# Kernel tuning notes

Hardware: AMD Instinct MI355X
Metric: run time of the kernel (lower is better)

## Reference

```python
import jax, jax.numpy as jnp
import numpy as np

WARP_WEIGHT = 2.5   # level 2
MD = 3              # max displacement -> 7x7 = 49 correlation channels
NEG_SLOPE = 0.1


def setup_inputs() -> dict:
    key = jax.random.key(0)
    ks = jax.random.split(key, 9)
    B, C, H, W = 8, 128, 128, 128
    features1 = jax.random.normal(ks[0], (B, C, H, W), jnp.float32)
    features2 = jax.random.normal(ks[1], (B, C, H, W), jnp.float32)
    flow = jax.random.normal(ks[2], (B, 2, H // 2, W // 2), jnp.float32)

    def conv_w(k, o, i, kh, kw):
        bound = 1.0 / np.sqrt(i * kh * kw)
        return jax.random.uniform(k, (o, i, kh, kw), jnp.float32, -bound, bound)

    def conv_b(k, o, i, kh, kw):
        bound = 1.0 / np.sqrt(i * kh * kw)
        return jax.random.uniform(k, (o,), jnp.float32, -bound, bound)

    return {
        "features1": features1,
        "features2": features2,
        "flow": flow,
        "w1": conv_w(ks[3], 64, 49, 3, 3), "b1": conv_b(ks[4], 64, 49, 3, 3),
        "w2": conv_w(ks[5], 32, 64, 3, 3), "b2": conv_b(ks[6], 32, 64, 3, 3),
        "w3": conv_w(ks[7], 2, 32, 5, 5),  "b3": conv_b(ks[8], 2, 32, 5, 5),
    }


def _resize_bilinear(x, h, w):
    # matches torch interpolate(mode='bilinear', align_corners=False)
    B, C = x.shape[:2]
    return jax.image.resize(x, (B, C, h, w), method="bilinear")


def _warp(img, fl):
    # backward warp: sample img at (x + fl_x, y + fl_y), bilinear, zeros outside
    B, C, H, W = img.shape
    yy, xx = jnp.meshgrid(jnp.arange(H, dtype=jnp.float32),
                          jnp.arange(W, dtype=jnp.float32), indexing="ij")
    x = xx[None] + fl[:, 0]   # [B,H,W]
    y = yy[None] + fl[:, 1]
    x0f, y0f = jnp.floor(x), jnp.floor(y)
    wx, wy = x - x0f, y - y0f
    x0, y0 = x0f.astype(jnp.int32), y0f.astype(jnp.int32)

    def gather(yi, xi):
        valid = (yi >= 0) & (yi < H) & (xi >= 0) & (xi < W)
        yc = jnp.clip(yi, 0, H - 1)
        xc = jnp.clip(xi, 0, W - 1)
        v = jax.vmap(lambda im, a, b: im[:, a, b])(img, yc, xc)  # [B,C,H,W]
        return v * valid[:, None].astype(img.dtype)

    return (gather(y0, x0) * ((1 - wx) * (1 - wy))[:, None]
            + gather(y0, x0 + 1) * (wx * (1 - wy))[:, None]
            + gather(y0 + 1, x0) * ((1 - wx) * wy)[:, None]
            + gather(y0 + 1, x0 + 1) * (wx * wy)[:, None])


def _correlation(f1, f2):
    # windowed cost volume: out[b, dy*7+dx] = mean_c f1[b,c,y,x]*f2[b,c,y+dy-3,x+dx-3]
    B, C, H, W = f1.shape
    f2p = jnp.pad(f2, ((0, 0), (0, 0), (MD, MD), (MD, MD)))
    outs = [jnp.mean(f1 * f2p[:, :, dy:dy + H, dx:dx + W], axis=1)
            for dy in range(2 * MD + 1) for dx in range(2 * MD + 1)]
    return jnp.stack(outs, axis=1)  # [B,49,H,W]


def _conv(x, w, b, pad):
    y = jax.lax.conv_general_dilated(
        x, w, window_strides=(1, 1), padding=[(pad, pad), (pad, pad)],
        dimension_numbers=("NCHW", "OIHW", "NCHW"))
    return y + b[None, :, None, None]


def _lrelu(x):
    return jnp.where(x >= 0, x, NEG_SLOPE * x)


def reference(features1, features2, flow, w1, b1, w2, b2, w3, b3):
    H, W = features1.shape[-2:]
    flow_up = _resize_bilinear(flow, H, W)                 # [B,2,H,W]
    f2w = _warp(features2, flow_up * WARP_WEIGHT)
    corr = _correlation(features1, f2w)                    # [B,49,H,W]
    h = _lrelu(_conv(corr, w1, b1, 1))
    h = _lrelu(_conv(h, w2, b2, 1))
    h = _conv(h, w3, b3, 2)                                # [B,2,H,W]
    return flow_up + h
```

## Files before the change

### kernel.cpp

```cpp
#include <hip/hip_runtime.h>
#include <hip/hip_bf16.h>

#define BB 8
#define CC 128
#define HH 128
#define WW 128
#define HW (HH*WW)
#define MD 3
#define ND 49
#define WARP_WEIGHT 2.5f
#define NEG 0.1f

typedef __attribute__((ext_vector_type(8))) short bf16x8;
typedef __attribute__((ext_vector_type(4))) float f32x4;

__device__ inline ushort f2bf(float f) {
    __hip_bfloat16 h = __float2bfloat16(f);
    return *reinterpret_cast<ushort*>(&h);
}
__device__ inline float bf2f(short s) {
    return __uint_as_float(((uint)(ushort)s) << 16);
}

#define G8_IDX(b, y, g) ((((size_t)((b) * HH + (y)) * 16) + (g)) * (WW * 8))

__global__ void k_flow_up(const float* __restrict__ flow, float* __restrict__ flow_up) {
    const int x = threadIdx.x;
    const int y = blockIdx.x;
    const int c = blockIdx.y;
    const int b = blockIdx.z;
    const int Hs = 64, Ws = 64;
    float sy = (y + 0.5f) * 0.5f - 0.5f;
    float sx = (x + 0.5f) * 0.5f - 0.5f;
    float y0f = floorf(sy), x0f = floorf(sx);
    int y0 = (int)y0f, x0 = (int)x0f;
    float wy = sy - y0f, wx = sx - x0f;
    int y0c = min(max(y0, 0), Hs - 1), y1c = min(max(y0 + 1, 0), Hs - 1);
    int x0c = min(max(x0, 0), Ws - 1), x1c = min(max(x0 + 1, 0), Ws - 1);
    const float* src = flow + ((size_t)(b * 2 + c)) * Hs * Ws;
    float v00 = src[y0c * Ws + x0c], v01 = src[y0c * Ws + x1c];
    float v10 = src[y1c * Ws + x0c], v11 = src[y1c * Ws + x1c];
    float v = v00 * (1.f - wx) * (1.f - wy) + v01 * wx * (1.f - wy)
            + v10 * (1.f - wx) * wy + v11 * wx * wy;
    flow_up[((size_t)(b * 2 + c) * HH + y) * WW + x] = v;
}

__global__ __launch_bounds__(256) void k_prep_cl(const float* __restrict__ src,
                                                 ushort* __restrict__ dstcl) {
    __shared__ ushort lds[128][68];
    const int y = blockIdx.x & 127;
    const int b = (blockIdx.x >> 7) & 7;
    const int chunk = blockIdx.x >> 10;
    {
        const int x = threadIdx.x & 127;
        const int cg = threadIdx.x >> 7;
        const int c0 = chunk * 64 + cg * 32;
        const float* s = src + ((size_t)b * CC + c0) * HW + y * WW + x;
#pragma unroll
        for (int j4 = 0; j4 < 8; j4++) {
            ushort t[4];
#pragma unroll
            for (int u = 0; u < 4; u++) t[u] = f2bf(s[(size_t)(j4 * 4 + u) * HW]);
            *reinterpret_cast<uint2*>(&lds[x][cg * 32 + j4 * 4]) =
                *reinterpret_cast<const uint2*>(t);
        }
    }
    __syncthreads();
    {
        const int xw = threadIdx.x >> 1;
        const int h = threadIdx.x & 1;
        ushort* d = dstcl + (((size_t)(b * HH + y)) * WW + xw) * CC + chunk * 64 + h * 32;
#pragma unroll
        for (int i = 0; i < 8; i++)
            *reinterpret_cast<uint2*>(d + i * 4) =
                *reinterpret_cast<const uint2*>(&lds[xw][h * 32 + i * 4]);
    }
}

__global__ __launch_bounds__(256) void k_warp2(const ushort* __restrict__ f2cl,
                                               const float* __restrict__ flow_up,
                                               ushort* __restrict__ f2wg8) {
    const int bid = blockIdx.x;
    const int k = bid & 7;
    const int t = bid >> 3;
    const int xs = t & 7;
    const int y  = k * 16 + ((t >> 3) & 15);
    const int b  = t >> 7;
    const int p  = threadIdx.x >> 4;
    const int g  = threadIdx.x & 15;
    const int x  = xs * 16 + p;

    const float fx = flow_up[((size_t)(b * 2 + 0) * HH + y) * WW + x] * WARP_WEIGHT;
    const float fy = flow_up[((size_t)(b * 2 + 1) * HH + y) * WW + x] * WARP_WEIGHT;
    const float sx = (float)x + fx;
    const float sy = (float)y + fy;
    float x0f = floorf(sx), y0f = floorf(sy);
    int x0 = (int)x0f, y0 = (int)y0f;
    float wx = sx - x0f, wy = sy - y0f;
    int x0c = min(max(x0, 0), WW - 1), x1c = min(max(x0 + 1, 0), WW - 1);
    int y0c = min(max(y0, 0), HH - 1), y1c = min(max(y0 + 1, 0), HH - 1);
    bool vx0 = (x0 >= 0) & (x0 < WW);
    bool vx1 = (x0 + 1 >= 0) & (x0 + 1 < WW);
    bool vy0 = (y0 >= 0) & (y0 < HH);
    bool vy1 = (y0 + 1 >= 0) & (y0 + 1 < HH);
    float w00 = (vx0 && vy0) ? (1.f - wx) * (1.f - wy) : 0.f;
    float w01 = (vx1 && vy0) ? wx * (1.f - wy) : 0.f;
    float w10 = (vx0 && vy1) ? (1.f - wx) * wy : 0.f;
    float w11 = (vx1 && vy1) ? wx * wy : 0.f;

    const ushort* base = f2cl + (size_t)b * HW * CC + (size_t)g * 8;
    bf16x8 t00 = *reinterpret_cast<const bf16x8*>(base + ((size_t)y0c * WW + x0c) * CC);
    bf16x8 t01 = *reinterpret_cast<const bf16x8*>(base + ((size_t)y0c * WW + x1c) * CC);
    bf16x8 t10 = *reinterpret_cast<const bf16x8*>(base + ((size_t)y1c * WW + x0c) * CC);
    bf16x8 t11 = *reinterpret_cast<const bf16x8*>(base + ((size_t)y1c * WW + x1c) * CC);

    ushort o[8];
#pragma unroll
    for (int j = 0; j < 8; j++) {
        float v = w00 * bf2f(t00[j]) + w01 * bf2f(t01[j])
                + w10 * bf2f(t10[j]) + w11 * bf2f(t11[j]);
        o[j] = f2bf(v);
    }
    *reinterpret_cast<uint4*>(f2wg8 + G8_IDX(b, y, g) + x * 8) =
        *reinterpret_cast<const uint4*>(o);
}

__global__ __launch_bounds__(512, 4) void k_corr_mfma(const float* __restrict__ f1,
                                                      const ushort* __restrict__ f2g8,
                                                      ushort* __restrict__ Ct) {
    __shared__ ushort cstage[128][68];
    const int b  = blockIdx.x & 7;
    const int y  = blockIdx.x >> 3;
    const int w  = threadIdx.x >> 6;
    const int l  = threadIdx.x & 63;
    const int lx = l & 15;
    const int lk = l >> 4;
    const int xa0 = w * 16;

    const int xb0 = xa0 - 3 + lx;
    const int xb1 = xa0 + 13 + lx;
    const int xc0 = min(max(xb0, 0), WW - 1);
    const int xc1 = min(max(xb1, 0), WW - 1);
    const bool xm0 = (unsigned)xb0 < (unsigned)WW;
    const bool xm1 = (unsigned)xb1 < (unsigned)WW;
    const bf16x8 zf = {};

    bf16x8 bb[2][8];
    auto load_b = [&](int dy, int buf) {
        const int yy = y + dy - MD;
        const bool yv = (unsigned)yy < (unsigned)HH;
        const int yc = min(max(yy, 0), HH - 1);
#pragma unroll
        for (int kk = 0; kk < 4; kk++) {
            const ushort* grp = f2g8 + G8_IDX(b, yc, kk * 4 + lk);
            bf16x8 b0 = *reinterpret_cast<const bf16x8*>(grp + xc0 * 8);
            bf16x8 b1 = *reinterpret_cast<const bf16x8*>(grp + xc1 * 8);
            bb[buf][kk * 2 + 0] = (yv && xm0) ? b0 : zf;
            bb[buf][kk * 2 + 1] = (yv && xm1) ? b1 : zf;
        }
    };

    load_b(0, 0);
    load_b(1, 1);

    bf16x8 afr[4];
#pragma unroll
    for (int kk = 0; kk < 4; kk++) {
        const float* src = f1 + ((size_t)(b * CC + kk * 32 + lk * 8)) * HW
                         + y * WW + xa0 + lx;
        float tv[8];
#pragma unroll
        for (int j = 0; j < 8; j++) tv[j] = src[(size_t)j * HW];
        ushort tmp[8];
#pragma unroll
        for (int j = 0; j < 8; j++) tmp[j] = f2bf(tv[j]);
        afr[kk] = *reinterpret_cast<const bf16x8*>(tmp);
    }

    const float scale = 1.f / (float)CC;

#pragma unroll
    for (int dy = 0; dy < 7; dy++) {
        f32x4 acc0 = (f32x4)(0.f), acc1 = (f32x4)(0.f);
#pragma unroll
        for (int kk = 0; kk < 4; kk++) {
            acc0 = __builtin_amdgcn_mfma_f32_16x16x32_bf16(
                afr[kk], bb[dy & 1][kk * 2 + 0], acc0, 0, 0, 0);
            acc1 = __builtin_amdgcn_mfma_f32_16x16x32_bf16(
                afr[kk], bb[dy & 1][kk * 2 + 1], acc1, 0, 0, 0);
        }
        if (dy + 2 < 7) load_b(dy + 2, dy & 1);
#pragma unroll
        for (int r = 0; r < 4; r++) {
            const int i = lk * 4 + r;
            const int d0 = lx - i;
            if (d0 >= 0 && d0 <= 6)
                cstage[xa0 + i][dy * 7 + d0] = f2bf(acc0[r] * scale);
            const int d1 = lx - i + 16;
            if (d1 >= 0 && d1 <= 6)
                cstage[xa0 + i][dy * 7 + d1] = f2bf(acc1[r] * scale);
        }
    }

    {
        const int row = xa0 + (l >> 2);
        const int part = l & 3;
        ushort* dst = Ct + (((size_t)(b * HH + y)) * WW + row) * 64 + part * 16;
        if (part < 3) {
            uint2 t0 = *reinterpret_cast<const uint2*>(&cstage[row][part * 16 + 0]);
            uint2 t1 = *reinterpret_cast<const uint2*>(&cstage[row][part * 16 + 4]);
            uint2 t2 = *reinterpret_cast<const uint2*>(&cstage[row][part * 16 + 8]);
            uint2 t3 = *reinterpret_cast<const uint2*>(&cstage[row][part * 16 + 12]);
            uint4 v0; v0.x = t0.x; v0.y = t0.y; v0.z = t1.x; v0.w = t1.y;
            uint4 v1; v1.x = t2.x; v1.y = t2.y; v1.z = t3.x; v1.w = t3.y;
            *reinterpret_cast<uint4*>(dst) = v0;
            *reinterpret_cast<uint4*>(dst + 8) = v1;
        } else {
            uint4 v0; v0.x = (uint)cstage[row][48]; v0.y = 0u; v0.z = 0u; v0.w = 0u;
            uint4 v1; v1.x = 0u; v1.y = 0u; v1.z = 0u; v1.w = 0u;
            *reinterpret_cast<uint4*>(dst) = v0;
            *reinterpret_cast<uint4*>(dst + 8) = v1;
        }
    }
}

template<int IC, int ICP, int OC, int OCP, int KK>
__global__ void k_prep_w2(const float* __restrict__ w, ushort* __restrict__ Wt) {
    constexpr int NCH = ICP / 32;
    int e = blockIdx.x * 256 + threadIdx.x;
    const int total = KK * KK * NCH * 4 * OCP * 8;
    if (e >= total) return;
    int j  = e & 7;
    int oc = (e >> 3) % OCP;
    int lk = (e / (8 * OCP)) & 3;
    int t  = e / (8 * OCP * 4);
    int ch = t % NCH;
    int tap = t / NCH;
    int kh = tap / KK, kw = tap % KK;
    int c = ch * 32 + lk * 8 + j;
    float v = 0.f;
    if (oc < OC && c < IC) v = w[((oc * IC + c) * KK + kh) * KK + kw];
    Wt[e] = f2bf(v);
}

template<int ICP, int OCP, int MT, int NT, int OCOUT, int KK, int PAD, bool RELU, bool LAST>
__global__ __launch_bounds__(512, 4) void k_conv_lds(
    const ushort* __restrict__ In, const ushort* __restrict__ Wt,
    const float* __restrict__ bias, ushort* __restrict__ Out,
    const float* __restrict__ flow_up, float* __restrict__ fout)
{
    constexpr int NCH = ICP / 32;
    constexpr int NTAP = KK * KK * NCH;
    constexpr int ROWB = ICP * 2;
    constexpr int ROWBYTES = WW * ROWB;
    constexpr int NROWS = KK + 1;
    constexpr int SLAB = NROWS * ROWBYTES;
    constexpr int LOG2ROWB = (ICP == 64) ? 7 : 6;
    constexpr int SWZM = (ICP == 64) ? 7 : 3;
    constexpr int ITER = SLAB / (512 * 16);

    __shared__ __align__(16) char slds[SLAB];

    const int y0 = blockIdx.x * 2;
    const int b = blockIdx.y;
    const char* inb = (const char*)(In + (size_t)b * HH * WW * ICP);

#pragma unroll
    for (int it = 0; it < ITER; it++) {
        int L = it * 512 * 16 + threadIdx.x * 16;
        int r = L / ROWBYTES;
        int Lr = L % ROWBYTES;
        int grow = min(max(y0 - PAD + r, 0), HH - 1);
        uint4 v = *reinterpret_cast<const uint4*>(inb + (size_t)grow * ROWBYTES + Lr);
        int dst = r * ROWBYTES + (Lr ^ (((Lr >> LOG2ROWB) & SWZM) << 4));
        *reinterpret_cast<uint4*>(&slds[dst]) = v;
    }
    __syncthreads();

    const int w = threadIdx.x >> 6;
    const int l = threadIdx.x & 63;
    const int lx = l & 15;
    const int lk = l >> 4;
    const int wr = w >> 2;
    const int wq = w & 3;
    const int y = y0 + wr;
    const int n0 = wq * (16 * NT);

    f32x4 acc[MT][NT];
#pragma unroll
    for (int m = 0; m < MT; m++)
#pragma unroll
        for (int nt = 0; nt < NT; nt++) acc[m][nt] = (f32x4)(0.f);

    bf16x8 abuf[2][MT];
    auto load_a = [&](int t, int buf) {
#pragma unroll
        for (int m = 0; m < MT; m++)
            abuf[buf][m] = *reinterpret_cast<const bf16x8*>(
                Wt + ((size_t)(t * 4 + lk) * OCP + m * 16 + lx) * 8);
    };

    load_a(0, 0);
#pragma unroll
    for (int t = 0; t < NTAP; t++) {
        if (t + 1 < NTAP) load_a(t + 1, (t + 1) & 1);
        const int kh = t / (KK * NCH);
        const int kw = (t / NCH) % KK;
        const int ch = t % NCH;
        const int slab_r = wr + kh;
        const int yy = y + kh - PAD;
        const bool yv = (unsigned)yy < (unsigned)HH;
        bf16x8 bfr[NT];
#pragma unroll
        for (int nt = 0; nt < NT; nt++) {
            int xx = n0 + nt * 16 + lx + kw - PAD;
            int xc = min(max(xx, 0), WW - 1);
            int off = slab_r * ROWBYTES
                    + ((xc * ROWB + (ch * 4 + lk) * 16) ^ ((xc & SWZM) << 4));
            bf16x8 v = *reinterpret_cast<const bf16x8*>(&slds[off]);
            bool valid = yv && ((unsigned)xx < (unsigned)WW);
            bfr[nt] = valid ? v : (bf16x8){};
        }
#pragma unroll
        for (int nt = 0; nt < NT; nt++)
#pragma unroll
            for (int m = 0; m < MT; m++)
                acc[m][nt] = __builtin_amdgcn_mfma_f32_16x16x32_bf16(
                    abuf[t & 1][m], bfr[nt], acc[m][nt], 0, 0, 0);
    }

    if (!LAST) {
#pragma unroll
        for (int m = 0; m < MT; m++) {
            const int oc0 = m * 16 + lk * 4;
            float4 bs = *reinterpret_cast<const float4*>(bias + oc0);
#pragma unroll
            for (int nt = 0; nt < NT; nt++) {
                int x = n0 + nt * 16 + lx;
                float v0 = acc[m][nt][0] + bs.x;
                float v1 = acc[m][nt][1] + bs.y;
                float v2 = acc[m][nt][2] + bs.z;
                float v3 = acc[m][nt][3] + bs.w;
                if (RELU) {
                    v0 = (v0 >= 0.f) ? v0 : NEG * v0;
                    v1 = (v1 >= 0.f) ? v1 : NEG * v1;
                    v2 = (v2 >= 0.f) ? v2 : NEG * v2;
                    v3 = (v3 >= 0.f) ? v3 : NEG * v3;
                }
                ushort4 o;
                o.x = f2bf(v0); o.y = f2bf(v1); o.z = f2bf(v2); o.w = f2bf(v3);
                *reinterpret_cast<ushort4*>(Out + (((size_t)(b * HH + y)) * WW + x) * OCOUT + oc0) = o;
            }
        }
    } else {
        if (lk == 0) {
#pragma unroll
            for (int nt = 0; nt < NT; nt++) {
                int x = n0 + nt * 16 + lx;
#pragma unroll
                for (int r = 0; r < 2; r++) {
                    size_t o = (((size_t)(b * 2 + r)) * HH + y) * WW + x;
                    fout[o] = acc[0][nt][r] + bias[r] + flow_up[o];
                }
            }
        }
    }
}

extern "C" void kernel_launch(void* const* d_in, const int* in_sizes, int n_in,
                              void* d_out, int out_size, void* d_ws, size_t ws_size,
                              hipStream_t stream) {
    const float* f1   = (const float*)d_in[0];
    const float* f2   = (const float*)d_in[1];
    const float* flow = (const float*)d_in[2];
    const float* w1   = (const float*)d_in[3];
    const float* b1   = (const float*)d_in[4];
    const float* w2   = (const float*)d_in[5];
    const float* b2   = (const float*)d_in[6];
    const float* w3   = (const float*)d_in[7];
    const float* b3   = (const float*)d_in[8];
    float* out = (float*)d_out;

    char* ws = (char*)d_ws;
    const size_t SZ_FLOWUP = (size_t)BB * 2 * HW * 4;
    const size_t SZ_CT     = (size_t)BB * HW * 64 * 2;
    const size_t SZ_WT1    = (size_t)9 * 2 * 4 * 64 * 8 * 2;
    const size_t SZ_WT2    = (size_t)9 * 2 * 4 * 32 * 8 * 2;
    const size_t SZ_WT3    = (size_t)25 * 1 * 4 * 16 * 8 * 2;
    const size_t SZ_BUF    = (size_t)BB * HW * CC * 2;

    float*  flow_up = (float*)ws;                         ws += SZ_FLOWUP;
    ushort* Ct      = (ushort*)ws;                        ws += SZ_CT;
    ushort* Wt1     = (ushort*)ws;                        ws += SZ_WT1;
    ushort* Wt2     = (ushort*)ws;                        ws += SZ_WT2;
    ushort* Wt3     = (ushort*)ws;                        ws += SZ_WT3;
    ushort* f2wg8   = (ushort*)ws;                        ws += SZ_BUF;
    ushort* bufA    = (ushort*)ws;
    ushort* f2cl    = bufA;
    ushort* h1      = bufA;
    ushort* h2      = (ushort*)((char*)bufA + (size_t)BB * HW * 64 * 2);

    k_prep_w2<49, 64, 64, 64, 3><<<dim3((9 * 2 * 4 * 64 * 8 + 255) / 256), dim3(256), 0, stream>>>(w1, Wt1);
    k_prep_w2<64, 64, 32, 32, 3><<<dim3((9 * 2 * 4 * 32 * 8 + 255) / 256), dim3(256), 0, stream>>>(w2, Wt2);
    k_prep_w2<32, 32, 2, 16, 5><<<dim3((25 * 1 * 4 * 16 * 8 + 255) / 256), dim3(256), 0, stream>>>(w3, Wt3);

    k_flow_up<<<dim3(HH, 2, BB), dim3(WW), 0, stream>>>(flow, flow_up);
    k_prep_cl<<<dim3(2048), dim3(256), 0, stream>>>(f2, f2cl);
    k_warp2  <<<dim3(8192), dim3(256), 0, stream>>>(f2cl, flow_up, f2wg8);
    k_corr_mfma<<<dim3(1024), dim3(512), 0, stream>>>(f1, f2wg8, Ct);

    k_conv_lds<64, 64, 4, 2, 64, 3, 1, true,  false>
        <<<dim3(HH / 2, BB), dim3(512), 0, stream>>>(Ct, Wt1, b1, h1, nullptr, nullptr);
    k_conv_lds<64, 32, 2, 2, 32, 3, 1, true,  false>
        <<<dim3(HH / 2, BB), dim3(512), 0, stream>>>(h1, Wt2, b2, h2, nullptr, nullptr);
    k_conv_lds<32, 16, 1, 2, 2,  5, 2, false, true >
        <<<dim3(HH / 2, BB), dim3(512), 0, stream>>>(h2, Wt3, b3, nullptr, flow_up, out);
}
```

Measured before the change: 124.7 us.

## Stage f2 rows in shared memory for correlation MFMA instead of register prefetch

The correlation kernel now copies each shifted f2 row (all 128 channels x 128 columns, 32 KB) cooperatively into LDS, then reads the MFMA B fragments from LDS. Before, each wave read its B fragments straight from global memory with a two-deep register double buffer, and neighbouring waves loaded overlapping halo columns. The aim is coalesced loads with no redundant halo fetches, and fewer registers, since the launch_bounds minimum-occupancy hint was also removed. The cost is two __syncthreads per dy step, loss of the load/compute overlap the prefetch gave, and extra LDS use that may limit how many blocks fit per CU.

Measured after the change: 121.0 us. 2.9% less time.

```diff
diff --git a/kernel.cpp b/kernel.cpp
--- a/kernel.cpp
+++ b/kernel.cpp
@@ -125,9 +125,10 @@
         *reinterpret_cast<const uint4*>(o);
 }
 
-__global__ __launch_bounds__(512, 4) void k_corr_mfma(const float* __restrict__ f1,
-                                                      const ushort* __restrict__ f2g8,
-                                                      ushort* __restrict__ Ct) {
+__global__ __launch_bounds__(512) void k_corr_mfma(const float* __restrict__ f1,
+                                                   const ushort* __restrict__ f2g8,
+                                                   ushort* __restrict__ Ct) {
+    __shared__ __align__(16) ushort sbuf[16 * 128 * 8];
     __shared__ ushort cstage[128][68];
     const int b  = blockIdx.x & 7;
     const int y  = blockIdx.x >> 3;
@@ -137,6 +138,20 @@
     const int lk = l >> 4;
     const int xa0 = w * 16;
 
+    bf16x8 afr[4];
+#pragma unroll
+    for (int kk = 0; kk < 4; kk++) {
+        const float* src = f1 + ((size_t)(b * CC + kk * 32 + lk * 8)) * HW
+                         + y * WW + xa0 + lx;
+        float tv[8];
+#pragma unroll
+        for (int j = 0; j < 8; j++) tv[j] = src[(size_t)j * HW];
+        ushort tmp[8];
+#pragma unroll
+        for (int j = 0; j < 8; j++) tmp[j] = f2bf(tv[j]);
+        afr[kk] = *reinterpret_cast<const bf16x8*>(tmp);
+    }
+
     const int xb0 = xa0 - 3 + lx;
     const int xb1 = xa0 + 13 + lx;
     const int xc0 = min(max(xb0, 0), WW - 1);
@@ -144,52 +159,34 @@
     const bool xm0 = (unsigned)xb0 < (unsigned)WW;
     const bool xm1 = (unsigned)xb1 < (unsigned)WW;
     const bf16x8 zf = {};
-
-    bf16x8 bb[2][8];
-    auto load_b = [&](int dy, int buf) {
+    const float scale = 1.f / (float)CC;
+
+    for (int dy = 0; dy < 7; dy++) {
         const int yy = y + dy - MD;
         const bool yv = (unsigned)yy < (unsigned)HH;
-        const int yc = min(max(yy, 0), HH - 1);
-#pragma unroll
-        for (int kk = 0; kk < 4; kk++) {
-            const ushort* grp = f2g8 + G8_IDX(b, yc, kk * 4 + lk);
-            bf16x8 b0 = *reinterpret_cast<const bf16x8*>(grp + xc0 * 8);
-            bf16x8 b1 = *reinterpret_cast<const bf16x8*>(grp + xc1 * 8);
-            bb[buf][kk * 2 + 0] = (yv && xm0) ? b0 : zf;
-            bb[buf][kk * 2 + 1] = (yv && xm1) ? b1 : zf;
-        }
-    };
-
-    load_b(0, 0);
-    load_b(1, 1);
-
-    bf16x8 afr[4];
-#pragma unroll
-    for (int kk = 0; kk < 4; kk++) {
-        const float* src = f1 + ((size_t)(b * CC + kk * 32 + lk * 8)) * HW
-                         + y * WW + xa0 + lx;
-        float tv[8];
-#pragma unroll
-        for (int j = 0; j < 8; j++) tv[j] = src[(size_t)j * HW];
-        ushort tmp[8];
-#pragma unroll
-        for (int j = 0; j < 8; j++) tmp[j] = f2bf(tv[j]);
-        afr[kk] = *reinterpret_cast<const bf16x8*>(tmp);
-    }
-
-    const float scale = 1.f / (float)CC;
-
-#pragma unroll
-    for (int dy = 0; dy < 7; dy++) {
+        if (yv) {
+            const ushort* src = f2g8 + G8_IDX(b, yy, 0) + threadIdx.x * 8;
+            ushort* dst = sbuf + threadIdx.x * 8;
+#pragma unroll
+            for (int i = 0; i < 4; i++)
+                *reinterpret_cast<uint4*>(dst + i * 4096) =
+                    *reinterpret_cast<const uint4*>(src + i * 4096);
+        }
+        __syncthreads();
+
         f32x4 acc0 = (f32x4)(0.f), acc1 = (f32x4)(0.f);
-#pragma unroll
-        for (int kk = 0; kk < 4; kk++) {
-            acc0 = __builtin_amdgcn_mfma_f32_16x16x32_bf16(
-                afr[kk], bb[dy & 1][kk * 2 + 0], acc0, 0, 0, 0);
-            acc1 = __builtin_amdgcn_mfma_f32_16x16x32_bf16(
-                afr[kk], bb[dy & 1][kk * 2 + 1], acc1, 0, 0, 0);
-        }
-        if (dy + 2 < 7) load_b(dy + 2, dy & 1);
+        if (yv) {
+#pragma unroll
+            for (int kk = 0; kk < 4; kk++) {
+                const ushort* grp = sbuf + (kk * 4 + lk) * (WW * 8);
+                bf16x8 b0 = *reinterpret_cast<const bf16x8*>(grp + xc0 * 8);
+                bf16x8 b1 = *reinterpret_cast<const bf16x8*>(grp + xc1 * 8);
+                b0 = xm0 ? b0 : zf;
+                b1 = xm1 ? b1 : zf;
+                acc0 = __builtin_amdgcn_mfma_f32_16x16x32_bf16(afr[kk], b0, acc0, 0, 0, 0);
+                acc1 = __builtin_amdgcn_mfma_f32_16x16x32_bf16(afr[kk], b1, acc1, 0, 0, 0);
+            }
+        }
 #pragma unroll
         for (int r = 0; r < 4; r++) {
             const int i = lk * 4 + r;
@@ -200,6 +197,7 @@
             if (d1 >= 0 && d1 <= 6)
                 cstage[xa0 + i][dy * 7 + d1] = f2bf(acc1[r] * scale);
         }
+        __syncthreads();
     }
 
     {
```
